# Kernel tuning notes

Hardware: AMD Instinct MI355X
Metric: run time of the kernel (lower is better)

The kernel has to match this reference:

```python
import jax, jax.numpy as jnp
import numpy as np

N_NODES = 50000
N_EDGES = 640000
HIDDEN = 128


def setup_inputs() -> dict:
    key = jax.random.key(0)
    ks = jax.random.split(key, 8)
    z = jax.random.normal(ks[0], (N_NODES, HIDDEN), dtype=jnp.float32)
    sources = jax.random.randint(ks[1], (N_EDGES,), 0, N_NODES)
    dists = jax.random.randint(ks[2], (N_EDGES,), 0, N_NODES)
    weights = jax.random.uniform(ks[3], (N_EDGES, 1), dtype=jnp.float32)
    # nn.Linear-style params: W has shape [out, in]; we store transposed [in, out]
    s_msg = 1.0 / np.sqrt(2 * HIDDEN + 1)
    W_msg = jax.random.uniform(ks[4], (2 * HIDDEN + 1, HIDDEN), minval=-s_msg, maxval=s_msg, dtype=jnp.float32)
    b_msg = jax.random.uniform(ks[5], (HIDDEN,), minval=-s_msg, maxval=s_msg, dtype=jnp.float32)
    s_upd = 1.0 / np.sqrt(2 * HIDDEN)
    W_upd = jax.random.uniform(ks[6], (2 * HIDDEN, HIDDEN), minval=-s_upd, maxval=s_upd, dtype=jnp.float32)
    b_upd = jax.random.uniform(ks[7], (HIDDEN,), minval=-s_upd, maxval=s_upd, dtype=jnp.float32)
    return {"z": z, "sources": sources, "dists": dists, "weights": weights,
            "W_msg": W_msg, "b_msg": b_msg, "W_upd": W_upd, "b_upd": b_upd}


def reference(z, sources, dists, weights, W_msg, b_msg, W_upd, b_upd):
    n = z.shape[0]
    # gather -> concat -> message linear: [E, 2h+1] @ [2h+1, h]
    msg_input = jnp.concatenate([z[sources], z[dists], weights], axis=1)
    messages = msg_input @ W_msg + b_msg
    # scatter-amax aggregate into node buffers (empty nodes -> -inf -> 0)
    agg = jax.ops.segment_max(messages, dists, num_segments=n)
    agg = jnp.where(jnp.isinf(agg), 0.0, agg)
    # update linear on [n, 2h]
    return jnp.concatenate([z, agg], axis=1) @ W_upd + b_upd
```

## Files before the change

### kernel.cpp

```cpp
#include <hip/hip_runtime.h>

#define H 128
#define KSLOT 64
#define CSTRIDE 16

typedef __attribute__((ext_vector_type(8))) short bf8;
typedef __attribute__((ext_vector_type(8))) unsigned short u16x8;
typedef __attribute__((ext_vector_type(4))) float f32x4;

__device__ __forceinline__ unsigned short f2bf(float f) {
    unsigned u = __float_as_uint(f);
    return (unsigned short)((u + 0x7FFFu + ((u >> 16) & 1u)) >> 16);
}
__device__ __forceinline__ float bf2f(unsigned short b) {
    return __uint_as_float(((unsigned)b) << 16);
}
__device__ __forceinline__ bf8 pack_bf8_from_f32(const float* p) {
    bf8 r;
#pragma unroll
    for (int i = 0; i < 8; ++i) r[i] = (short)f2bf(p[i]);
    return r;
}

__global__ __launch_bounds__(256) void prep(
    const float* __restrict__ Wmsg, const float* __restrict__ Wupd,
    unsigned short* __restrict__ WmT,
    unsigned short* __restrict__ WuT,
    int* __restrict__ cnt,
    unsigned short* __restrict__ ZS,
    int N)
{
    const int t = blockIdx.x * 256 + threadIdx.x;
    const int n4 = (N * CSTRIDE) >> 2;
    if (t < n4) ((int4*)cnt)[t] = make_int4(0, 0, 0, 0);
    if (t < 16) {
        u16x8 s;
#pragma unroll
        for (int i = 0; i < 8; ++i) s[i] = 0xFF80;
        *(u16x8*)(ZS + (size_t)N * H + t * 8) = s;
    }
    if (t < 256 * H) {
        const int c = t >> 7, k = t & 127;
        WmT[t] = f2bf(Wmsg[(size_t)(k + (c & 128)) * H + (c & 127)]);
    }
    if (t < H * 256) {
        const int c = t >> 8, k = t & 255;
        WuT[t] = f2bf(Wupd[(size_t)k * H + c]);
    }
}

__global__ __launch_bounds__(256) void gemm1_scatter(
    const float* __restrict__ z,
    const unsigned short* __restrict__ WmT,
    unsigned short* __restrict__ ZS,
    unsigned short* __restrict__ ZD,
    const int* __restrict__ src, const int* __restrict__ dst,
    const float* __restrict__ wgt, int* __restrict__ cnt,
    int2* __restrict__ ew,
    int N, int E, int ntiles, int ngemm)
{
    if ((int)blockIdx.x >= ngemm) {
        const int base = (blockIdx.x - ngemm) * 1024 + threadIdx.x;
        int dv[4], sv[4]; float wv[4]; bool ok[4];
#pragma unroll
        for (int k = 0; k < 4; ++k) {
            const int e = base + k * 256;
            ok[k] = e < E;
            const int ec = ok[k] ? e : 0;
            dv[k] = dst[ec]; sv[k] = src[ec]; wv[k] = wgt[ec];
        }
#pragma unroll
        for (int k = 0; k < 4; ++k) {
            if (ok[k]) {
                int p = atomicAdd(&cnt[(size_t)dv[k] * CSTRIDE], 1);
                if (p < KSLOT)
                    ew[((size_t)dv[k] << 6) + p] = make_int2(sv[k], __float_as_int(wv[k]));
            }
        }
        return;
    }
    const int l = threadIdx.x & 63;
    const int w = threadIdx.x >> 6;
    const int r = l & 15, g = l >> 4;
    const int colbase = w * 64;
    unsigned short* Out = (w < 2) ? ZS : ZD;
    const int outcol = colbase & 127;

    bf8 wf[4][4];
#pragma unroll
    for (int nf = 0; nf < 4; ++nf)
#pragma unroll
        for (int kk = 0; kk < 4; ++kk)
            wf[kk][nf] = *(const bf8*)(WmT + (size_t)(colbase + nf * 16 + r) * H + kk * 32 + g * 8);

    const f32x4 zero = {0.f, 0.f, 0.f, 0.f};
    for (int tt = blockIdx.x; tt < ntiles; tt += ngemm) {
        const int row0 = tt * 32;
#pragma unroll
        for (int m = 0; m < 2; ++m) {
            const int node = row0 + m * 16 + r;
            const int rowc = node < N ? node : N - 1;
            bf8 zf[4];
#pragma unroll
            for (int kk = 0; kk < 4; ++kk)
                zf[kk] = pack_bf8_from_f32(z + (size_t)rowc * H + kk * 32 + g * 8);
            f32x4 acc[4] = {zero, zero, zero, zero};
#pragma unroll
            for (int kk = 0; kk < 4; ++kk)
#pragma unroll
                for (int nf = 0; nf < 4; ++nf)
                    acc[nf] = __builtin_amdgcn_mfma_f32_16x16x32_bf16(wf[kk][nf], zf[kk], acc[nf], 0, 0, 0);
            if (node < N) {
#pragma unroll
                for (int nf = 0; nf < 4; ++nf) {
                    ushort4 o;
                    o.x = f2bf(acc[nf][0]); o.y = f2bf(acc[nf][1]);
                    o.z = f2bf(acc[nf][2]); o.w = f2bf(acc[nf][3]);
                    *(ushort4*)(Out + (size_t)node * H + outcol + nf * 16 + g * 4) = o;
                }
            }
        }
    }
}

__global__ __launch_bounds__(256) void aggregate(
    const unsigned short* __restrict__ ZS,
    const unsigned short* __restrict__ ZD,
    unsigned short* __restrict__ Agg,
    const float* __restrict__ bmsg, const float* __restrict__ wrow,
    const int* __restrict__ cnt, const int2* __restrict__ ew, int N)
{
    const int node = blockIdx.x * 4 + (threadIdx.x >> 6);
    if (node >= N) return;
    const int l = threadIdx.x & 63;
    const int sub = l >> 4;
    const int c16 = l & 15;

    const int d = min(cnt[(size_t)node * CSTRIDE], KSLOT);
    const int iters = (d + 7) >> 3;

    float wr[8];
    {
        float4 w0 = *(const float4*)(wrow + c16 * 8);
        float4 w1 = *(const float4*)(wrow + c16 * 8 + 4);
        wr[0] = w0.x; wr[1] = w0.y; wr[2] = w0.z; wr[3] = w0.w;
        wr[4] = w1.x; wr[5] = w1.y; wr[6] = w1.z; wr[7] = w1.w;
    }

    const float NINF = -__builtin_inff();
    float m[8];
#pragma unroll
    for (int i = 0; i < 8; ++i) m[i] = NINF;

    const int2* ep = ew + ((size_t)node << 6) + sub;
    for (int j = 0; j < iters; ++j) {
        const int s0 = j * 8 + sub, s1 = s0 + 4;
        int2 e0 = ep[j * 8];
        int2 e1 = ep[j * 8 + 4];
        const int r0 = (s0 < d) ? e0.x : N;
        const int r1 = (s1 < d) ? e1.x : N;
        const float w0 = (s0 < d) ? __int_as_float(e0.y) : 0.f;
        const float w1 = (s1 < d) ? __int_as_float(e1.y) : 0.f;
        u16x8 v0 = *(const u16x8*)(ZS + (size_t)r0 * H + c16 * 8);
        u16x8 v1 = *(const u16x8*)(ZS + (size_t)r1 * H + c16 * 8);
#pragma unroll
        for (int i = 0; i < 8; ++i)
            m[i] = fmaxf(m[i], __builtin_fmaf(w0, wr[i], bf2f((unsigned short)v0[i])));
#pragma unroll
        for (int i = 0; i < 8; ++i)
            m[i] = fmaxf(m[i], __builtin_fmaf(w1, wr[i], bf2f((unsigned short)v1[i])));
    }
#pragma unroll
    for (int i = 0; i < 8; ++i) {
        m[i] = fmaxf(m[i], __shfl_xor(m[i], 16));
        m[i] = fmaxf(m[i], __shfl_xor(m[i], 32));
    }

    if (sub == 0) {
        u16x8 zd = *(const u16x8*)(ZD + (size_t)node * H + c16 * 8);
        float bm[8];
        float4 b0 = *(const float4*)(bmsg + c16 * 8);
        float4 b1 = *(const float4*)(bmsg + c16 * 8 + 4);
        bm[0] = b0.x; bm[1] = b0.y; bm[2] = b0.z; bm[3] = b0.w;
        bm[4] = b1.x; bm[5] = b1.y; bm[6] = b1.z; bm[7] = b1.w;
        u16x8 o;
#pragma unroll
        for (int i = 0; i < 8; ++i) {
            float r = (d > 0) ? (m[i] + bf2f((unsigned short)zd[i]) + bm[i]) : 0.f;
            o[i] = f2bf(r);
        }
        *(u16x8*)(Agg + (size_t)node * H + c16 * 8) = o;
    }
}

__global__ __launch_bounds__(256) void gemm_upd_mfma(
    const float* __restrict__ z,
    const unsigned short* __restrict__ Agg,
    const unsigned short* __restrict__ WuT,
    const float* __restrict__ bupd,
    float* __restrict__ out, int N, int ntiles)
{
    const int l = threadIdx.x & 63;
    const int w = threadIdx.x >> 6;
    const int r = l & 15, g = l >> 4;
    const int colbase = w * 32;

    bf8 wf[8][2];
#pragma unroll
    for (int nf = 0; nf < 2; ++nf)
#pragma unroll
        for (int kk = 0; kk < 8; ++kk)
            wf[kk][nf] = *(const bf8*)(WuT + (size_t)(colbase + nf * 16 + r) * 256 + kk * 32 + g * 8);
    float4 bias[2];
#pragma unroll
    for (int nf = 0; nf < 2; ++nf)
        bias[nf] = *(const float4*)(bupd + colbase + nf * 16 + g * 4);

    const f32x4 zero = {0.f, 0.f, 0.f, 0.f};
    for (int tt = blockIdx.x; tt < ntiles; tt += gridDim.x) {
        const int row0 = tt * 32;
#pragma unroll
        for (int m = 0; m < 2; ++m) {
            const int node = row0 + m * 16 + r;
            const int rowc = node < N ? node : N - 1;
            bf8 zf[8];
#pragma unroll
            for (int kk = 0; kk < 4; ++kk)
                zf[kk] = pack_bf8_from_f32(z + (size_t)rowc * H + kk * 32 + g * 8);
#pragma unroll
            for (int kk = 4; kk < 8; ++kk)
                zf[kk] = *(const bf8*)(Agg + (size_t)rowc * H + (kk - 4) * 32 + g * 8);
            f32x4 acc[2] = {zero, zero};
#pragma unroll
            for (int kk = 0; kk < 8; ++kk)
#pragma unroll
                for (int nf = 0; nf < 2; ++nf)
                    acc[nf] = __builtin_amdgcn_mfma_f32_16x16x32_bf16(wf[kk][nf], zf[kk], acc[nf], 0, 0, 0);
            if (node < N) {
#pragma unroll
                for (int nf = 0; nf < 2; ++nf) {
                    float4 o;
                    o.x = acc[nf][0] + bias[nf].x;
                    o.y = acc[nf][1] + bias[nf].y;
                    o.z = acc[nf][2] + bias[nf].z;
                    o.w = acc[nf][3] + bias[nf].w;
                    *(float4*)(out + (size_t)node * H + colbase + nf * 16 + g * 4) = o;
                }
            }
        }
    }
}

extern "C" void kernel_launch(void* const* d_in, const int* in_sizes, int n_in,
                              void* d_out, int out_size, void* d_ws, size_t ws_size,
                              hipStream_t stream) {
    const float* z    = (const float*)d_in[0];
    const int*   src  = (const int*)d_in[1];
    const int*   dst  = (const int*)d_in[2];
    const float* wgt  = (const float*)d_in[3];
    const float* Wmsg = (const float*)d_in[4];
    const float* bmsg = (const float*)d_in[5];
    const float* Wupd = (const float*)d_in[6];
    const float* bupd = (const float*)d_in[7];
    float* out = (float*)d_out;

    const int N = in_sizes[0] / H;
    const int E = in_sizes[1];
    const int Npad = ((N + 31) / 32) * 32;
    const int ntiles = Npad / 32;

    unsigned short* ZS  = (unsigned short*)d_ws;
    unsigned short* ZD  = ZS + (size_t)(Npad + 32) * H;
    unsigned short* Agg = ZD + (size_t)Npad * H;
    unsigned short* WmT = Agg + (size_t)Npad * H;
    unsigned short* WuT = WmT + 256 * H;
    int*  cnt = (int*)(WuT + H * 256);
    int2* ew  = (int2*)(cnt + (size_t)N * CSTRIDE);

    const int ngemm = 784;
    const int nscat = (E + 1023) / 1024;
    const int nprep = ((N * CSTRIDE / 4) + 255) / 256;

    prep<<<nprep, 256, 0, stream>>>(Wmsg, Wupd, WmT, WuT, cnt, ZS, N);

    gemm1_scatter<<<ngemm + nscat, 256, 0, stream>>>(
        z, WmT, ZS, ZD, src, dst, wgt, cnt, ew, N, E, ntiles, ngemm);

    aggregate<<<(N + 3) / 4, 256, 0, stream>>>(
        ZS, ZD, Agg, bmsg, Wmsg + (size_t)256 * H, cnt, ew, N);

    gemm_upd_mfma<<<784, 256, 0, stream>>>(z, Agg, WuT, bupd, out, N, ntiles);
}
```

Before: 134.3 us.

## Fuse aggregation into update GEMM via LDS and pre-convert z to bf16 once

The segment-max aggregation and the update GEMM become one kernel. Each block aggregates 32 nodes into shared memory and then runs the MFMA update on those rows, so the Agg buffer no longer makes a round trip through global memory and one launch is removed. z is also converted to bf16 once in the prep kernel, so both GEMMs read a half-size bf16 copy instead of converting fp32 on the fly. The trade-offs are an extra full pass over z in prep, fewer threads in flight during the latency-bound gather phase (8 nodes per wave, serial), and weight-fragment reloads per block instead of a persistent grid.

Result: faster. 129.9 us (-3.3%).

```diff
diff --git a/kernel.cpp b/kernel.cpp
--- a/kernel.cpp
+++ b/kernel.cpp
@@ -15,15 +15,10 @@
 __device__ __forceinline__ float bf2f(unsigned short b) {
     return __uint_as_float(((unsigned)b) << 16);
 }
-__device__ __forceinline__ bf8 pack_bf8_from_f32(const float* p) {
-    bf8 r;
-#pragma unroll
-    for (int i = 0; i < 8; ++i) r[i] = (short)f2bf(p[i]);
-    return r;
-}
 
 __global__ __launch_bounds__(256) void prep(
-    const float* __restrict__ Wmsg, const float* __restrict__ Wupd,
+    const float* __restrict__ z, const float* __restrict__ Wmsg, const float* __restrict__ Wupd,
+    unsigned short* __restrict__ zb,
     unsigned short* __restrict__ WmT,
     unsigned short* __restrict__ WuT,
     int* __restrict__ cnt,
@@ -33,6 +28,16 @@
     const int t = blockIdx.x * 256 + threadIdx.x;
     const int n4 = (N * CSTRIDE) >> 2;
     if (t < n4) ((int4*)cnt)[t] = make_int4(0, 0, 0, 0);
+    const int zi = t * 8;
+    if (zi < N * H) {
+        const float4* p = (const float4*)(z + zi);
+        float4 v0 = p[0], v1 = p[1];
+        ushort4 o0, o1;
+        o0.x = f2bf(v0.x); o0.y = f2bf(v0.y); o0.z = f2bf(v0.z); o0.w = f2bf(v0.w);
+        o1.x = f2bf(v1.x); o1.y = f2bf(v1.y); o1.z = f2bf(v1.z); o1.w = f2bf(v1.w);
+        ushort4* q = (ushort4*)(zb + zi);
+        q[0] = o0; q[1] = o1;
+    }
     if (t < 16) {
         u16x8 s;
 #pragma unroll
@@ -50,7 +55,7 @@
 }
 
 __global__ __launch_bounds__(256) void gemm1_scatter(
-    const float* __restrict__ z,
+    const unsigned short* __restrict__ zb,
     const unsigned short* __restrict__ WmT,
     unsigned short* __restrict__ ZS,
     unsigned short* __restrict__ ZD,
@@ -103,7 +108,7 @@
             bf8 zf[4];
 #pragma unroll
             for (int kk = 0; kk < 4; ++kk)
-                zf[kk] = pack_bf8_from_f32(z + (size_t)rowc * H + kk * 32 + g * 8);
+                zf[kk] = *(const bf8*)(zb + (size_t)rowc * H + kk * 32 + g * 8);
             f32x4 acc[4] = {zero, zero, zero, zero};
 #pragma unroll
             for (int kk = 0; kk < 4; ++kk)
@@ -123,102 +128,99 @@
     }
 }
 
-__global__ __launch_bounds__(256) void aggregate(
+__global__ __launch_bounds__(256) void agg_gemm2(
+    const unsigned short* __restrict__ zb,
     const unsigned short* __restrict__ ZS,
     const unsigned short* __restrict__ ZD,
-    unsigned short* __restrict__ Agg,
+    const unsigned short* __restrict__ WuT,
     const float* __restrict__ bmsg, const float* __restrict__ wrow,
-    const int* __restrict__ cnt, const int2* __restrict__ ew, int N)
+    const float* __restrict__ bupd,
+    const int* __restrict__ cnt, const int2* __restrict__ ew,
+    float* __restrict__ out, int N)
 {
-    const int node = blockIdx.x * 4 + (threadIdx.x >> 6);
-    if (node >= N) return;
-    const int l = threadIdx.x & 63;
-    const int sub = l >> 4;
-    const int c16 = l & 15;
-
-    const int d = min(cnt[(size_t)node * CSTRIDE], KSLOT);
-    const int iters = (d + 7) >> 3;
-
-    float wr[8];
-    {
-        float4 w0 = *(const float4*)(wrow + c16 * 8);
-        float4 w1 = *(const float4*)(wrow + c16 * 8 + 4);
-        wr[0] = w0.x; wr[1] = w0.y; wr[2] = w0.z; wr[3] = w0.w;
-        wr[4] = w1.x; wr[5] = w1.y; wr[6] = w1.z; wr[7] = w1.w;
-    }
-
-    const float NINF = -__builtin_inff();
-    float m[8];
-#pragma unroll
-    for (int i = 0; i < 8; ++i) m[i] = NINF;
-
-    const int2* ep = ew + ((size_t)node << 6) + sub;
-    for (int j = 0; j < iters; ++j) {
-        const int s0 = j * 8 + sub, s1 = s0 + 4;
-        int2 e0 = ep[j * 8];
-        int2 e1 = ep[j * 8 + 4];
-        const int r0 = (s0 < d) ? e0.x : N;
-        const int r1 = (s1 < d) ? e1.x : N;
-        const float w0 = (s0 < d) ? __int_as_float(e0.y) : 0.f;
-        const float w1 = (s1 < d) ? __int_as_float(e1.y) : 0.f;
-        u16x8 v0 = *(const u16x8*)(ZS + (size_t)r0 * H + c16 * 8);
-        u16x8 v1 = *(const u16x8*)(ZS + (size_t)r1 * H + c16 * 8);
-#pragma unroll
-        for (int i = 0; i < 8; ++i)
-            m[i] = fmaxf(m[i], __builtin_fmaf(w0, wr[i], bf2f((unsigned short)v0[i])));
-#pragma unroll
-        for (int i = 0; i < 8; ++i)
-            m[i] = fmaxf(m[i], __builtin_fmaf(w1, wr[i], bf2f((unsigned short)v1[i])));
-    }
-#pragma unroll
-    for (int i = 0; i < 8; ++i) {
-        m[i] = fmaxf(m[i], __shfl_xor(m[i], 16));
-        m[i] = fmaxf(m[i], __shfl_xor(m[i], 32));
-    }
-
-    if (sub == 0) {
-        u16x8 zd = *(const u16x8*)(ZD + (size_t)node * H + c16 * 8);
-        float bm[8];
-        float4 b0 = *(const float4*)(bmsg + c16 * 8);
-        float4 b1 = *(const float4*)(bmsg + c16 * 8 + 4);
-        bm[0] = b0.x; bm[1] = b0.y; bm[2] = b0.z; bm[3] = b0.w;
-        bm[4] = b1.x; bm[5] = b1.y; bm[6] = b1.z; bm[7] = b1.w;
-        u16x8 o;
-#pragma unroll
-        for (int i = 0; i < 8; ++i) {
-            float r = (d > 0) ? (m[i] + bf2f((unsigned short)zd[i]) + bm[i]) : 0.f;
-            o[i] = f2bf(r);
-        }
-        *(u16x8*)(Agg + (size_t)node * H + c16 * 8) = o;
-    }
-}
-
-__global__ __launch_bounds__(256) void gemm_upd_mfma(
-    const float* __restrict__ z,
-    const unsigned short* __restrict__ Agg,
-    const unsigned short* __restrict__ WuT,
-    const float* __restrict__ bupd,
-    float* __restrict__ out, int N, int ntiles)
-{
+    __shared__ unsigned short aggl[32][144];
+
     const int l = threadIdx.x & 63;
     const int w = threadIdx.x >> 6;
-    const int r = l & 15, g = l >> 4;
-    const int colbase = w * 32;
-
-    bf8 wf[8][2];
-#pragma unroll
-    for (int nf = 0; nf < 2; ++nf)
-#pragma unroll
-        for (int kk = 0; kk < 8; ++kk)
-            wf[kk][nf] = *(const bf8*)(WuT + (size_t)(colbase + nf * 16 + r) * 256 + kk * 32 + g * 8);
-    float4 bias[2];
-#pragma unroll
-    for (int nf = 0; nf < 2; ++nf)
-        bias[nf] = *(const float4*)(bupd + colbase + nf * 16 + g * 4);
-
-    const f32x4 zero = {0.f, 0.f, 0.f, 0.f};
-    for (int tt = blockIdx.x; tt < ntiles; tt += gridDim.x) {
-        const int row0 = tt * 32;
+    const int row0 = blockIdx.x * 32;
+
+    {
+        const int sub = l >> 4;
+        const int c16 = l & 15;
+        float wr[8], bm[8];
+        {
+            float4 w0 = *(const float4*)(wrow + c16 * 8);
+            float4 w1 = *(const float4*)(wrow + c16 * 8 + 4);
+            wr[0] = w0.x; wr[1] = w0.y; wr[2] = w0.z; wr[3] = w0.w;
+            wr[4] = w1.x; wr[5] = w1.y; wr[6] = w1.z; wr[7] = w1.w;
+            float4 b0 = *(const float4*)(bmsg + c16 * 8);
+            float4 b1 = *(const float4*)(bmsg + c16 * 8 + 4);
+            bm[0] = b0.x; bm[1] = b0.y; bm[2] = b0.z; bm[3] = b0.w;
+            bm[4] = b1.x; bm[5] = b1.y; bm[6] = b1.z; bm[7] = b1.w;
+        }
+        const float NINF = -__builtin_inff();
+        for (int i = 0; i < 8; ++i) {
+            const int nodeLocal = w * 8 + i;
+            const int node = row0 + nodeLocal;
+            if (node < N) {
+                const int d = min(cnt[(size_t)node * CSTRIDE], KSLOT);
+                const int iters = (d + 7) >> 3;
+                float m[8];
+#pragma unroll
+                for (int q = 0; q < 8; ++q) m[q] = NINF;
+                const int2* ep = ew + ((size_t)node << 6) + sub;
+                for (int j = 0; j < iters; ++j) {
+                    const int s0 = j * 8 + sub, s1 = s0 + 4;
+                    int2 e0 = ep[j * 8];
+                    int2 e1 = ep[j * 8 + 4];
+                    const int r0 = (s0 < d) ? e0.x : N;
+                    const int r1 = (s1 < d) ? e1.x : N;
+                    const float w0 = (s0 < d) ? __int_as_float(e0.y) : 0.f;
+                    const float w1 = (s1 < d) ? __int_as_float(e1.y) : 0.f;
+                    u16x8 v0 = *(const u16x8*)(ZS + (size_t)r0 * H + c16 * 8);
+                    u16x8 v1 = *(const u16x8*)(ZS + (size_t)r1 * H + c16 * 8);
+#pragma unroll
+                    for (int q = 0; q < 8; ++q)
+                        m[q] = fmaxf(m[q], __builtin_fmaf(w0, wr[q], bf2f((unsigned short)v0[q])));
+#pragma unroll
+                    for (int q = 0; q < 8; ++q)
+                        m[q] = fmaxf(m[q], __builtin_fmaf(w1, wr[q], bf2f((unsigned short)v1[q])));
+                }
+#pragma unroll
+                for (int q = 0; q < 8; ++q) {
+                    m[q] = fmaxf(m[q], __shfl_xor(m[q], 16));
+                    m[q] = fmaxf(m[q], __shfl_xor(m[q], 32));
+                }
+                if (sub == 0) {
+                    u16x8 zd = *(const u16x8*)(ZD + (size_t)node * H + c16 * 8);
+                    u16x8 o;
+#pragma unroll
+                    for (int q = 0; q < 8; ++q) {
+                        float rv = (d > 0) ? (m[q] + bf2f((unsigned short)zd[q]) + bm[q]) : 0.f;
+                        o[q] = f2bf(rv);
+                    }
+                    *(u16x8*)(&aggl[nodeLocal][c16 * 8]) = o;
+                }
+            }
+        }
+    }
+    __syncthreads();
+
+    {
+        const int r = l & 15, g = l >> 4;
+        const int colbase = w * 32;
+        bf8 wf[8][2];
+#pragma unroll
+        for (int nf = 0; nf < 2; ++nf)
+#pragma unroll
+            for (int kk = 0; kk < 8; ++kk)
+                wf[kk][nf] = *(const bf8*)(WuT + (size_t)(colbase + nf * 16 + r) * 256 + kk * 32 + g * 8);
+        float4 bias[2];
+#pragma unroll
+        for (int nf = 0; nf < 2; ++nf)
+            bias[nf] = *(const float4*)(bupd + colbase + nf * 16 + g * 4);
+
+        const f32x4 zero = {0.f, 0.f, 0.f, 0.f};
 #pragma unroll
         for (int m = 0; m < 2; ++m) {
             const int node = row0 + m * 16 + r;
@@ -226,10 +228,10 @@
             bf8 zf[8];
 #pragma unroll
             for (int kk = 0; kk < 4; ++kk)
-                zf[kk] = pack_bf8_from_f32(z + (size_t)rowc * H + kk * 32 + g * 8);
+                zf[kk] = *(const bf8*)(zb + (size_t)rowc * H + kk * 32 + g * 8);
 #pragma unroll
             for (int kk = 4; kk < 8; ++kk)
-                zf[kk] = *(const bf8*)(Agg + (size_t)rowc * H + (kk - 4) * 32 + g * 8);
+                zf[kk] = *(const bf8*)(&aggl[m * 16 + r][(kk - 4) * 32 + g * 8]);
             f32x4 acc[2] = {zero, zero};
 #pragma unroll
             for (int kk = 0; kk < 8; ++kk)
@@ -269,25 +271,24 @@
     const int Npad = ((N + 31) / 32) * 32;
     const int ntiles = Npad / 32;
 
-    unsigned short* ZS  = (unsigned short*)d_ws;
+    unsigned short* zb  = (unsigned short*)d_ws;
+    unsigned short* ZS  = zb + (size_t)Npad * H;
     unsigned short* ZD  = ZS + (size_t)(Npad + 32) * H;
-    unsigned short* Agg = ZD + (size_t)Npad * H;
-    unsigned short* WmT = Agg + (size_t)Npad * H;
+    unsigned short* WmT = ZD + (size_t)Npad * H;
     unsigned short* WuT = WmT + 256 * H;
     int*  cnt = (int*)(WuT + H * 256);
     int2* ew  = (int2*)(cnt + (size_t)N * CSTRIDE);
 
     const int ngemm = 784;
     const int nscat = (E + 1023) / 1024;
-    const int nprep = ((N * CSTRIDE / 4) + 255) / 256;
-
-    prep<<<nprep, 256, 0, stream>>>(Wmsg, Wupd, WmT, WuT, cnt, ZS, N);
+    const int nprep_threads = max(N * H / 8, (N * CSTRIDE) / 4);
+    const int nprep = (nprep_threads + 255) / 256;
+
+    prep<<<nprep, 256, 0, stream>>>(z, Wmsg, Wupd, zb, WmT, WuT, cnt, ZS, N);
 
     gemm1_scatter<<<ngemm + nscat, 256, 0, stream>>>(
-        z, WmT, ZS, ZD, src, dst, wgt, cnt, ew, N, E, ntiles, ngemm);
-
-    aggregate<<<(N + 3) / 4, 256, 0, stream>>>(
-        ZS, ZD, Agg, bmsg, Wmsg + (size_t)256 * H, cnt, ew, N);
-
-    gemm_upd_mfma<<<784, 256, 0, stream>>>(z, Agg, WuT, bupd, out, N, ntiles);
-}
+        zb, WmT, ZS, ZD, src, dst, wgt, cnt, ew, N, E, ntiles, ngemm);
+
+    agg_gemm2<<<ntiles, 256, 0, stream>>>(
+        zb, ZS, ZD, WuT, bmsg, Wmsg + (size_t)256 * H, bupd, cnt, ew, out, N);
+}
```
